# Performance work log

Measured on AMD Instinct MI355X. Metric: run time of the kernel, lower is better.

Reference implementation:

```python
import jax, jax.numpy as jnp
import numpy as np

N_NODES = 100000
N_EDGES = 1600000
IN_C, HID, N_CLS = 128, 128, 40


def setup_inputs() -> dict:
    key = jax.random.key(0)
    ks = jax.random.split(key, 8)
    x = jax.random.normal(ks[0], (N_NODES, IN_C), dtype=jnp.float32)
    edge_index = jax.random.randint(ks[1], (2, N_EDGES), 0, N_NODES, dtype=jnp.int64)
    s1 = 1.0 / np.sqrt(IN_C)
    s2 = 1.0 / np.sqrt(HID)
    return {
        "x": x,
        "edge_index": edge_index,
        "Wl1": jax.random.normal(ks[2], (IN_C, HID), dtype=jnp.float32) * s1,
        "Wr1": jax.random.normal(ks[3], (IN_C, HID), dtype=jnp.float32) * s1,
        "b1": jnp.zeros((HID,), dtype=jnp.float32),
        "Wl2": jax.random.normal(ks[4], (HID, N_CLS), dtype=jnp.float32) * s2,
        "Wr2": jax.random.normal(ks[5], (HID, N_CLS), dtype=jnp.float32) * s2,
        "b2": jnp.zeros((N_CLS,), dtype=jnp.float32),
    }


def _sage_conv(x, src, dst, Wl, Wr, b):
    # mean-aggregate neighbor features at destination nodes
    n = x.shape[0]
    agg = jax.ops.segment_sum(x[src], dst, num_segments=n)           # [N, C]
    cnt = jax.ops.segment_sum(jnp.ones((src.shape[0],), x.dtype), dst, num_segments=n)
    mean = agg / jnp.maximum(cnt, 1.0)[:, None]
    return mean @ Wl + x @ Wr + b


def reference(x, edge_index, Wl1, Wr1, b1, Wl2, Wr2, b2):
    src, dst = edge_index[0], edge_index[1]
    h = jax.nn.relu(_sage_conv(x, src, dst, Wl1, Wr1, b1))
    return _sage_conv(h, src, dst, Wl2, Wr2, b2)
```

## Files before the change

kernel.cpp:

```cpp
#include <hip/hip_runtime.h>

#define C_IN 128
#define N_CLS 40
#define ZB   40

#define NPB   256
#define MAXNB 512
#define CAP   6144
#define BCSTR 16

typedef __attribute__((ext_vector_type(8))) short bf16x8;
typedef __attribute__((ext_vector_type(4))) float f32x4;
typedef __attribute__((ext_vector_type(2))) float f32x2;

__device__ __forceinline__ ushort f2b(float f) {
  union { float f; unsigned u; } v; v.f = f;
  unsigned r = v.u + 0x7FFF + ((v.u >> 16) & 1);
  return (ushort)(r >> 16);
}
__device__ __forceinline__ unsigned packbf(float lo, float hi) {
  return (unsigned)f2b(lo) | ((unsigned)f2b(hi) << 16);
}
__device__ __forceinline__ void acc2(float& fa, float& fb, unsigned u) {
  union { unsigned u; float f; } lo, hi;
  lo.u = u << 16; hi.u = u & 0xFFFF0000u;
  fa += lo.f; fb += hi.f;
}

#if __has_builtin(__builtin_amdgcn_cvt_pk_f32_fp8) && __has_builtin(__builtin_amdgcn_cvt_pk_fp8_f32)
#define HW_FP8 1
#else
#define HW_FP8 0
#endif

__device__ __forceinline__ float f8dec1(unsigned b) {
  unsigned E = (b >> 3) & 15, M = b & 7;
  if (E) {
    union { unsigned u; float f; } v;
    v.u = ((b & 0x80u) << 24) | ((E + 120u) << 23) | (M << 20);
    return v.f;
  }
  float m = (float)(int)M * 0.001953125f;
  return (b & 0x80u) ? -m : m;
}
__device__ __forceinline__ unsigned f8enc1(float x) {
  union { float f; unsigned u; } v; v.f = x;
  unsigned s = (v.u >> 31) << 7;
  float ax = fabsf(x);
  if (ax < 9.765625e-4f) return s;
  if (ax < 0.015625f) {
    int M = (int)rintf(ax * 512.0f);
    return (M >= 8) ? (s | 0x08u) : (s | (unsigned)M);
  }
  if (ax > 448.0f) return s | 0x7Eu;
  unsigned au = v.u & 0x7FFFFFFFu;
  unsigned r = au + 0x7FFFFu + ((au >> 20) & 1);
  int e = (int)(r >> 23) - 127;
  unsigned M = (r >> 20) & 7;
  if (e > 8) return s | 0x7Eu;
  return s | ((unsigned)(e + 7) << 3) | M;
}
__device__ __forceinline__ void accf8x4(float* a, unsigned u) {
#if HW_FP8
  f32x2 lo = __builtin_amdgcn_cvt_pk_f32_fp8((int)u, false);
  f32x2 hi = __builtin_amdgcn_cvt_pk_f32_fp8((int)u, true);
  a[0] += lo[0]; a[1] += lo[1]; a[2] += hi[0]; a[3] += hi[1];
#else
  a[0] += f8dec1(u & 0xFF); a[1] += f8dec1((u >> 8) & 0xFF);
  a[2] += f8dec1((u >> 16) & 0xFF); a[3] += f8dec1(u >> 24);
#endif
}
__device__ __forceinline__ unsigned packf8x4(float x0, float x1, float x2, float x3) {
#if HW_FP8
  int p = 0;
  p = __builtin_amdgcn_cvt_pk_fp8_f32(x0, x1, p, false);
  p = __builtin_amdgcn_cvt_pk_fp8_f32(x2, x3, p, true);
  return (unsigned)p;
#else
  return f8enc1(x0) | (f8enc1(x1) << 8) | (f8enc1(x2) << 16) | (f8enc1(x3) << 24);
#endif
}
__device__ __forceinline__ unsigned char f8enc_byte(float x) {
#if HW_FP8
  return (unsigned char)(__builtin_amdgcn_cvt_pk_fp8_f32(x, x, 0, false) & 0xFF);
#else
  return (unsigned char)f8enc1(x);
#endif
}

__global__ __launch_bounds__(256) void bin_kernel(
    const int* __restrict__ src, const int* __restrict__ dst,
    int* __restrict__ bcur, unsigned* __restrict__ staged, int E, int NB)
{
  __shared__ int wcnt[4][MAXNB];
  __shared__ int wbase[4][MAXNB];
  const int tid = threadIdx.x;
  const int wv = tid >> 6;
  for (int i = tid; i < NB; i += 256) {
    wcnt[0][i] = 0; wcnt[1][i] = 0; wcnt[2][i] = 0; wcnt[3][i] = 0;
  }
  __syncthreads();
  const int e0 = blockIdx.x * 2048;
  const int eend = min(e0 + 2048, E);
  for (int e = e0 + tid; e < eend; e += 256)
    atomicAdd(&wcnt[wv][dst[e] >> 8], 1);
  __syncthreads();
  for (int i = tid; i < NB; i += 256) {
    int c0 = wcnt[0][i], c1 = wcnt[1][i], c2 = wcnt[2][i], c3 = wcnt[3][i];
    int tot = c0 + c1 + c2 + c3;
    int g = (tot > 0) ? atomicAdd(&bcur[i * BCSTR], tot) : 0;
    wbase[0][i] = g;
    wbase[1][i] = g + c0;
    wbase[2][i] = g + c0 + c1;
    wbase[3][i] = g + c0 + c1 + c2;
    wcnt[0][i] = 0; wcnt[1][i] = 0; wcnt[2][i] = 0; wcnt[3][i] = 0;
  }
  __syncthreads();
  for (int e = e0 + tid; e < eend; e += 256) {
    int d = dst[e];
    int b = d >> 8;
    int pos = wbase[wv][b] + atomicAdd(&wcnt[wv][b], 1);
    if (pos < CAP)
      staged[(size_t)b * CAP + pos] = (unsigned)src[e] | ((unsigned)(d & 255) << 20);
  }
}

__global__ __launch_bounds__(256) void csr_cvt_kernel(
    const unsigned* __restrict__ staged, const int* __restrict__ bcur,
    int* __restrict__ row_ptr, int* __restrict__ deg, int* __restrict__ csr_src,
    int N, int NB,
    const float* __restrict__ xin, ushort* __restrict__ xb,
    unsigned char* __restrict__ xf8, long n8)
{
  __shared__ unsigned st[CAP];
  __shared__ int dcnt[NPB];
  __shared__ int cur[NPB];
  __shared__ int wsum[4];
  __shared__ int rb_s;
  const int tid = threadIdx.x;
  if (blockIdx.x >= NB) {
    long i = ((long)(blockIdx.x - NB) * 256 + tid);
    if (i < n8) {
      const float4 a = *reinterpret_cast<const float4*>(xin + i * 8);
      const float4 b = *reinterpret_cast<const float4*>(xin + i * 8 + 4);
      uint4 o;
      o.x = packbf(a.x, a.y);
      o.y = packbf(a.z, a.w);
      o.z = packbf(b.x, b.y);
      o.w = packbf(b.z, b.w);
      *reinterpret_cast<uint4*>(xb + i * 8) = o;
      uint2 p;
      p.x = packf8x4(a.x, a.y, a.z, a.w);
      p.y = packf8x4(b.x, b.y, b.z, b.w);
      *reinterpret_cast<uint2*>(xf8 + i * 8) = p;
    }
    return;
  }
  const int b = blockIdx.x;
  const int cb = min(bcur[b * BCSTR], CAP);
  for (int i = tid; i < cb; i += 256) st[i] = staged[(size_t)b * CAP + i];
  int part = 0;
  for (int i = tid; i < b; i += 256) part += min(bcur[i * BCSTR], CAP);
  if (tid == 0) rb_s = 0;
  dcnt[tid] = 0;
  __syncthreads();
  #pragma unroll
  for (int off = 32; off > 0; off >>= 1) part += __shfl_down(part, off);
  if ((tid & 63) == 0 && part != 0) atomicAdd(&rb_s, part);
  for (int i = tid; i < cb; i += 256) atomicAdd(&dcnt[st[i] >> 20], 1);
  __syncthreads();
  const int rb = rb_s;
  int d = dcnt[tid];
  const int lane = tid & 63, w = tid >> 6;
  int inc = d;
  #pragma unroll
  for (int off = 1; off < 64; off <<= 1) {
    int v = __shfl_up(inc, off);
    if (lane >= off) inc += v;
  }
  if (lane == 63) wsum[w] = inc;
  __syncthreads();
  int wo = 0;
  for (int i = 0; i < w; ++i) wo += wsum[i];
  const int excl = wo + inc - d;
  cur[tid] = excl;
  const int node = b * NPB + tid;
  if (node < N) { row_ptr[node] = rb + excl; deg[node] = d; }
  __syncthreads();
  for (int i = tid; i < cb; i += 256) {
    unsigned wv = st[i];
    int p = atomicAdd(&cur[wv >> 20], 1);
    csr_src[rb + p] = (int)(wv & 0xFFFFF);
  }
}

__global__ __launch_bounds__(256) void agg1_kernel(
    const unsigned char* __restrict__ xf8, const ushort* __restrict__ xb,
    const int* __restrict__ csr_src, const int* __restrict__ row_ptr,
    const int* __restrict__ deg, ushort* __restrict__ mean, int N)
{
  int t = blockIdx.x * 256 + threadIdx.x;
  int n = t >> 3;
  if (n >= N) return;
  int q = t & 7;
  int base = row_ptr[n];
  int d = deg[n];
  float a[16];
  #pragma unroll
  for (int i = 0; i < 16; ++i) a[i] = 0.f;
  if (d > 8) {
    const unsigned char* fq = xf8 + q * 16;
    int j = 0;
    for (; j + 4 <= d; j += 4) {
      int s0 = csr_src[base + j + 0];
      int s1 = csr_src[base + j + 1];
      int s2 = csr_src[base + j + 2];
      int s3 = csr_src[base + j + 3];
      uint4 v0 = *reinterpret_cast<const uint4*>(fq + (size_t)s0 * C_IN);
      uint4 v1 = *reinterpret_cast<const uint4*>(fq + (size_t)s1 * C_IN);
      uint4 v2 = *reinterpret_cast<const uint4*>(fq + (size_t)s2 * C_IN);
      uint4 v3 = *reinterpret_cast<const uint4*>(fq + (size_t)s3 * C_IN);
      accf8x4(a+0, v0.x); accf8x4(a+4, v0.y); accf8x4(a+8, v0.z); accf8x4(a+12, v0.w);
      accf8x4(a+0, v1.x); accf8x4(a+4, v1.y); accf8x4(a+8, v1.z); accf8x4(a+12, v1.w);
      accf8x4(a+0, v2.x); accf8x4(a+4, v2.y); accf8x4(a+8, v2.z); accf8x4(a+12, v2.w);
      accf8x4(a+0, v3.x); accf8x4(a+4, v3.y); accf8x4(a+8, v3.z); accf8x4(a+12, v3.w);
    }
    for (; j < d; ++j) {
      int s = csr_src[base + j];
      uint4 v = *reinterpret_cast<const uint4*>(fq + (size_t)s * C_IN);
      accf8x4(a+0, v.x); accf8x4(a+4, v.y); accf8x4(a+8, v.z); accf8x4(a+12, v.w);
    }
  } else {
    const ushort* fq = xb + q * 16;
    for (int j = 0; j < d; ++j) {
      int s = csr_src[base + j];
      uint4 w0 = *reinterpret_cast<const uint4*>(fq + (size_t)s * C_IN);
      uint4 w1 = *reinterpret_cast<const uint4*>(fq + (size_t)s * C_IN + 8);
      acc2(a[0],a[1],w0.x); acc2(a[2],a[3],w0.y); acc2(a[4],a[5],w0.z); acc2(a[6],a[7],w0.w);
      acc2(a[8],a[9],w1.x); acc2(a[10],a[11],w1.y); acc2(a[12],a[13],w1.z); acc2(a[14],a[15],w1.w);
    }
  }
  float inv = (d > 0) ? (1.0f / (float)d) : 0.0f;
  uint4 o0, o1;
  o0.x = packbf(a[0]*inv, a[1]*inv);  o0.y = packbf(a[2]*inv, a[3]*inv);
  o0.z = packbf(a[4]*inv, a[5]*inv);  o0.w = packbf(a[6]*inv, a[7]*inv);
  o1.x = packbf(a[8]*inv, a[9]*inv);  o1.y = packbf(a[10]*inv, a[11]*inv);
  o1.z = packbf(a[12]*inv, a[13]*inv); o1.w = packbf(a[14]*inv, a[15]*inv);
  uint4* mp = reinterpret_cast<uint4*>(mean + (size_t)n * C_IN + q * 16);
  mp[0] = o0;
  mp[1] = o1;
}

__global__ __launch_bounds__(256) void layer1_mfma(
    const ushort* __restrict__ xb, const ushort* __restrict__ mb,
    const float* __restrict__ Wr, const float* __restrict__ Wl,
    const float* __restrict__ bias, ushort* __restrict__ h, int N, int ntiles)
{
  __shared__ ushort sB[8 * 8 * 64 * 8];
  const int tid = threadIdx.x;
  for (int idx = tid; idx < 8 * 8 * 64; idx += 256) {
    int l  = idx & 63;
    int cg = (idx >> 6) & 7;
    int ks = idx >> 9;
    int c  = cg * 16 + (l & 15);
    int kb = ks * 32 + 8 * (l >> 4);
    ushort* p = &sB[idx * 8];
    #pragma unroll
    for (int j = 0; j < 8; ++j) {
      int k = kb + j;
      float w = (k < C_IN) ? Wr[k * C_IN + c] : Wl[(k - C_IN) * C_IN + c];
      p[j] = f2b(w);
    }
  }
  __syncthreads();
  const int w = tid >> 6, l = tid & 63;
  const int rfrag = l & 15, kg = l >> 4;
  for (int tile = blockIdx.x; tile < ntiles; tile += gridDim.x) {
    int n0 = tile * 128 + w * 32;
    int rc0 = n0 + rfrag;      rc0 = (rc0 < N) ? rc0 : (N - 1);
    int rc1 = n0 + 16 + rfrag; rc1 = (rc1 < N) ? rc1 : (N - 1);
    f32x4 acc[2][8] = {};
    #pragma unroll
    for (int ks = 0; ks < 8; ++ks) {
      int kb = ks * 32 + kg * 8;
      const ushort* Asrc = (kb < C_IN) ? (xb + kb) : (mb + (kb - C_IN));
      bf16x8 a0 = *reinterpret_cast<const bf16x8*>(Asrc + (size_t)rc0 * C_IN);
      bf16x8 a1 = *reinterpret_cast<const bf16x8*>(Asrc + (size_t)rc1 * C_IN);
      #pragma unroll
      for (int cg = 0; cg < 8; ++cg) {
        bf16x8 b = *reinterpret_cast<const bf16x8*>(&sB[((ks * 8 + cg) * 64 + l) * 8]);
        acc[0][cg] = __builtin_amdgcn_mfma_f32_16x16x32_bf16(a0, b, acc[0][cg], 0, 0, 0);
        acc[1][cg] = __builtin_amdgcn_mfma_f32_16x16x32_bf16(a1, b, acc[1][cg], 0, 0, 0);
      }
    }
    const int rowoff = (l >> 4) * 4, colbase = l & 15;
    #pragma unroll
    for (int f = 0; f < 2; ++f) {
      #pragma unroll
      for (int cg = 0; cg < 8; ++cg) {
        int c = cg * 16 + colbase;
        float bc = bias[c];
        #pragma unroll
        for (int r = 0; r < 4; ++r) {
          int row = n0 + f * 16 + rowoff + r;
          if (row < N) {
            float v = fmaxf(acc[f][cg][r] + bc, 0.0f);
            h[(size_t)row * C_IN + c] = f2b(v);
          }
        }
      }
    }
  }
}

__global__ __launch_bounds__(256) void gemm2_dual(
    const ushort* __restrict__ hb,
    const float* __restrict__ Wl, const float* __restrict__ Wr,
    unsigned char* __restrict__ z, float* __restrict__ out, int N, int ntiles)
{
  __shared__ ushort sBl[4 * 3 * 64 * 8];
  __shared__ ushort sBr[4 * 3 * 64 * 8];
  const int tid = threadIdx.x;
  for (int idx = tid; idx < 4 * 3 * 64; idx += 256) {
    int l  = idx & 63;
    int cg = (idx >> 6) % 3;
    int ks = idx / (3 * 64);
    int c  = cg * 16 + (l & 15);
    int kb = ks * 32 + 8 * (l >> 4);
    ushort* pl = &sBl[idx * 8];
    ushort* pr = &sBr[idx * 8];
    #pragma unroll
    for (int j = 0; j < 8; ++j) {
      int k = kb + j;
      float wl = 0.0f, wr = 0.0f;
      if (c < N_CLS) { wl = Wl[k * N_CLS + c]; wr = Wr[k * N_CLS + c]; }
      pl[j] = f2b(wl);
      pr[j] = f2b(wr);
    }
  }
  __syncthreads();
  const int w = tid >> 6, l = tid & 63;
  const int rfrag = l & 15, kg = l >> 4;
  for (int tile = blockIdx.x; tile < ntiles; tile += gridDim.x) {
    int n0 = tile * 128 + w * 32;
    int rc0 = n0 + rfrag;      rc0 = (rc0 < N) ? rc0 : (N - 1);
    int rc1 = n0 + 16 + rfrag; rc1 = (rc1 < N) ? rc1 : (N - 1);
    f32x4 az[2][3] = {};
    f32x4 ay[2][3] = {};
    #pragma unroll
    for (int ks = 0; ks < 4; ++ks) {
      int kb = ks * 32 + kg * 8;
      bf16x8 a0 = *reinterpret_cast<const bf16x8*>(hb + (size_t)rc0 * C_IN + kb);
      bf16x8 a1 = *reinterpret_cast<const bf16x8*>(hb + (size_t)rc1 * C_IN + kb);
      #pragma unroll
      for (int cg = 0; cg < 3; ++cg) {
        bf16x8 bl = *reinterpret_cast<const bf16x8*>(&sBl[((ks * 3 + cg) * 64 + l) * 8]);
        bf16x8 br = *reinterpret_cast<const bf16x8*>(&sBr[((ks * 3 + cg) * 64 + l) * 8]);
        az[0][cg] = __builtin_amdgcn_mfma_f32_16x16x32_bf16(a0, bl, az[0][cg], 0, 0, 0);
        az[1][cg] = __builtin_amdgcn_mfma_f32_16x16x32_bf16(a1, bl, az[1][cg], 0, 0, 0);
        ay[0][cg] = __builtin_amdgcn_mfma_f32_16x16x32_bf16(a0, br, ay[0][cg], 0, 0, 0);
        ay[1][cg] = __builtin_amdgcn_mfma_f32_16x16x32_bf16(a1, br, ay[1][cg], 0, 0, 0);
      }
    }
    const int rowoff = (l >> 4) * 4, colbase = l & 15;
    #pragma unroll
    for (int f = 0; f < 2; ++f) {
      #pragma unroll
      for (int cg = 0; cg < 3; ++cg) {
        int c = cg * 16 + colbase;
        if (c < N_CLS) {
          #pragma unroll
          for (int r = 0; r < 4; ++r) {
            int row = n0 + f * 16 + rowoff + r;
            if (row < N) {
              z[(size_t)row * ZB + c] = f8enc_byte(az[f][cg][r]);
              out[(size_t)row * N_CLS + c] = ay[f][cg][r];
            }
          }
        }
      }
    }
  }
}

__global__ __launch_bounds__(256) void agg2z_kernel(
    const unsigned char* __restrict__ z, const int* __restrict__ csr_src,
    const int* __restrict__ row_ptr, const int* __restrict__ deg,
    const float* __restrict__ b2, float* __restrict__ out, int N)
{
  unsigned w = blockIdx.x * 256 + threadIdx.x;
  unsigned n = w / 5u;
  if (n >= (unsigned)N) return;
  unsigned q = w - n * 5u;
  const unsigned char* zq = z + q * 8;
  int base = row_ptr[n];
  int d = deg[n];
  float a[8];
  #pragma unroll
  for (int i = 0; i < 8; ++i) a[i] = 0.f;
  int j = 0;
  for (; j + 4 <= d; j += 4) {
    int s0 = csr_src[base + j + 0];
    int s1 = csr_src[base + j + 1];
    int s2 = csr_src[base + j + 2];
    int s3 = csr_src[base + j + 3];
    uint2 v0 = *reinterpret_cast<const uint2*>(zq + (size_t)s0 * ZB);
    uint2 v1 = *reinterpret_cast<const uint2*>(zq + (size_t)s1 * ZB);
    uint2 v2 = *reinterpret_cast<const uint2*>(zq + (size_t)s2 * ZB);
    uint2 v3 = *reinterpret_cast<const uint2*>(zq + (size_t)s3 * ZB);
    accf8x4(a+0, v0.x); accf8x4(a+4, v0.y);
    accf8x4(a+0, v1.x); accf8x4(a+4, v1.y);
    accf8x4(a+0, v2.x); accf8x4(a+4, v2.y);
    accf8x4(a+0, v3.x); accf8x4(a+4, v3.y);
  }
  for (; j < d; ++j) {
    int s = csr_src[base + j];
    uint2 v = *reinterpret_cast<const uint2*>(zq + (size_t)s * ZB);
    accf8x4(a+0, v.x); accf8x4(a+4, v.y);
  }
  float inv = (d > 0) ? (1.0f / (float)d) : 0.0f;
  float* op = out + (size_t)n * N_CLS + q * 8;
  const float4 bA = *reinterpret_cast<const float4*>(b2 + q * 8);
  const float4 bB = *reinterpret_cast<const float4*>(b2 + q * 8 + 4);
  float4 y0 = *reinterpret_cast<const float4*>(op);
  float4 y1 = *reinterpret_cast<const float4*>(op + 4);
  y0.x += a[0] * inv + bA.x; y0.y += a[1] * inv + bA.y;
  y0.z += a[2] * inv + bA.z; y0.w += a[3] * inv + bA.w;
  y1.x += a[4] * inv + bB.x; y1.y += a[5] * inv + bB.y;
  y1.z += a[6] * inv + bB.z; y1.w += a[7] * inv + bB.w;
  *reinterpret_cast<float4*>(op) = y0;
  *reinterpret_cast<float4*>(op + 4) = y1;
}

extern "C" void kernel_launch(void* const* d_in, const int* in_sizes, int n_in,
                              void* d_out, int out_size, void* d_ws, size_t ws_size,
                              hipStream_t stream)
{
  const float* x   = (const float*)d_in[0];
  const int*   ei  = (const int*)d_in[1];
  const float* Wl1 = (const float*)d_in[2];
  const float* Wr1 = (const float*)d_in[3];
  const float* b1  = (const float*)d_in[4];
  const float* Wl2 = (const float*)d_in[5];
  const float* Wr2 = (const float*)d_in[6];
  const float* b2  = (const float*)d_in[7];
  float* out = (float*)d_out;

  const int N = in_sizes[0] / C_IN;
  const int E = in_sizes[1] / 2;
  const int* src = ei;
  const int* dst = ei + E;
  const int NB = (N + NPB - 1) / NPB;

  size_t Np = ((size_t)N + 255) & ~(size_t)255;
  size_t Ep = ((size_t)E + 255) & ~(size_t)255;
  int* wsi     = (int*)d_ws;
  int* bcur    = wsi;
  int* row_ptr = wsi + (size_t)MAXNB * BCSTR;
  int* deg     = row_ptr + Np;
  int* csr_src = deg + Np;
  unsigned* staged = (unsigned*)(csr_src + Ep);
  unsigned char* zb = (unsigned char*)staged;
  ushort* xb    = (ushort*)(staged + (size_t)MAXNB * CAP);
  ushort* meanb = xb + (size_t)N * C_IN;
  ushort* hb    = meanb + (size_t)N * C_IN;
  unsigned char* xf8 = (unsigned char*)(hb + (size_t)N * C_IN);

  hipMemsetAsync(bcur, 0, (size_t)MAXNB * BCSTR * sizeof(int), stream);

  const int nbin = (E + 2047) / 2048;
  bin_kernel<<<nbin, 256, 0, stream>>>(src, dst, bcur, staged, E, NB);

  long n8 = (long)N * C_IN / 8;
  const int ncvt = (int)((n8 + 255) / 256);
  csr_cvt_kernel<<<NB + ncvt, 256, 0, stream>>>(staged, bcur, row_ptr, deg, csr_src,
                                                N, NB, x, xb, xf8, n8);

  const int ntiles = (N + 127) / 128;

  agg1_kernel<<<(N * 8 + 255) / 256, 256, 0, stream>>>(xf8, xb, csr_src, row_ptr, deg, meanb, N);
  layer1_mfma<<<512, 256, 0, stream>>>(xb, meanb, Wr1, Wl1, b1, hb, N, ntiles);

  gemm2_dual<<<512, 256, 0, stream>>>(hb, Wl2, Wr2, zb, out, N, ntiles);
  agg2z_kernel<<<(N * 5 + 255) / 256, 256, 0, stream>>>(zb, csr_src, row_ptr, deg, b2, out, N);
}
```

Measured before the change: 188.5 us.

## Fuse x conversion into edge binning kernel and enlarge bin chunks

The bf16/fp8 conversion of x now runs in the same launch as the edge binning kernel rather than alongside CSR construction. Each binning block now handles 8192 edges instead of 2048, caches the packed edge words and bin ids in shared memory so dst/src are read only once, and uses one shared counter set instead of four per-wave sets. The goal is fewer global atomics on bcur, no second read of the edge arrays, and better overlap of the conversion work with the binning. In exchange there are fewer binning blocks, more shared-memory use per block, and more contention on the shared-memory atomics.

New measurement: 170.8 us. -9.4%, faster.

```diff
diff --git a/kernel.cpp b/kernel.cpp
--- a/kernel.cpp
+++ b/kernel.cpp
@@ -8,6 +8,7 @@
 #define MAXNB 512
 #define CAP   6144
 #define BCSTR 16
+#define BINB  8192
 
 typedef __attribute__((ext_vector_type(8))) short bf16x8;
 typedef __attribute__((ext_vector_type(4))) float f32x4;
@@ -88,58 +89,19 @@
 #endif
 }
 
-__global__ __launch_bounds__(256) void bin_kernel(
+__global__ __launch_bounds__(256) void bin_cvt_kernel(
     const int* __restrict__ src, const int* __restrict__ dst,
-    int* __restrict__ bcur, unsigned* __restrict__ staged, int E, int NB)
-{
-  __shared__ int wcnt[4][MAXNB];
-  __shared__ int wbase[4][MAXNB];
-  const int tid = threadIdx.x;
-  const int wv = tid >> 6;
-  for (int i = tid; i < NB; i += 256) {
-    wcnt[0][i] = 0; wcnt[1][i] = 0; wcnt[2][i] = 0; wcnt[3][i] = 0;
-  }
-  __syncthreads();
-  const int e0 = blockIdx.x * 2048;
-  const int eend = min(e0 + 2048, E);
-  for (int e = e0 + tid; e < eend; e += 256)
-    atomicAdd(&wcnt[wv][dst[e] >> 8], 1);
-  __syncthreads();
-  for (int i = tid; i < NB; i += 256) {
-    int c0 = wcnt[0][i], c1 = wcnt[1][i], c2 = wcnt[2][i], c3 = wcnt[3][i];
-    int tot = c0 + c1 + c2 + c3;
-    int g = (tot > 0) ? atomicAdd(&bcur[i * BCSTR], tot) : 0;
-    wbase[0][i] = g;
-    wbase[1][i] = g + c0;
-    wbase[2][i] = g + c0 + c1;
-    wbase[3][i] = g + c0 + c1 + c2;
-    wcnt[0][i] = 0; wcnt[1][i] = 0; wcnt[2][i] = 0; wcnt[3][i] = 0;
-  }
-  __syncthreads();
-  for (int e = e0 + tid; e < eend; e += 256) {
-    int d = dst[e];
-    int b = d >> 8;
-    int pos = wbase[wv][b] + atomicAdd(&wcnt[wv][b], 1);
-    if (pos < CAP)
-      staged[(size_t)b * CAP + pos] = (unsigned)src[e] | ((unsigned)(d & 255) << 20);
-  }
-}
-
-__global__ __launch_bounds__(256) void csr_cvt_kernel(
-    const unsigned* __restrict__ staged, const int* __restrict__ bcur,
-    int* __restrict__ row_ptr, int* __restrict__ deg, int* __restrict__ csr_src,
-    int N, int NB,
+    int* __restrict__ bcur, unsigned* __restrict__ staged, int E, int NB, int nbin,
     const float* __restrict__ xin, ushort* __restrict__ xb,
     unsigned char* __restrict__ xf8, long n8)
 {
-  __shared__ unsigned st[CAP];
-  __shared__ int dcnt[NPB];
-  __shared__ int cur[NPB];
-  __shared__ int wsum[4];
-  __shared__ int rb_s;
+  __shared__ unsigned sw[BINB];
+  __shared__ ushort  sb[BINB];
+  __shared__ int cnt[MAXNB];
+  __shared__ int base[MAXNB];
   const int tid = threadIdx.x;
-  if (blockIdx.x >= NB) {
-    long i = ((long)(blockIdx.x - NB) * 256 + tid);
+  if (blockIdx.x >= nbin) {
+    long i = ((long)(blockIdx.x - nbin) * 256 + tid);
     if (i < n8) {
       const float4 a = *reinterpret_cast<const float4*>(xin + i * 8);
       const float4 b = *reinterpret_cast<const float4*>(xin + i * 8 + 4);
@@ -156,7 +118,43 @@
     }
     return;
   }
-  const int b = blockIdx.x;
+  for (int i = tid; i < NB; i += 256) cnt[i] = 0;
+  __syncthreads();
+  const int e0 = blockIdx.x * BINB;
+  const int nE = min(BINB, E - e0);
+  for (int k = tid; k < nE; k += 256) {
+    int d = dst[e0 + k];
+    int s = src[e0 + k];
+    int b = d >> 8;
+    sw[k] = (unsigned)s | ((unsigned)(d & 255) << 20);
+    sb[k] = (ushort)b;
+    atomicAdd(&cnt[b], 1);
+  }
+  __syncthreads();
+  for (int i = tid; i < NB; i += 256) {
+    int c = cnt[i];
+    base[i] = (c > 0) ? atomicAdd(&bcur[i * BCSTR], c) : 0;
+    cnt[i] = 0;
+  }
+  __syncthreads();
+  for (int k = tid; k < nE; k += 256) {
+    int b = sb[k];
+    int pos = base[b] + atomicAdd(&cnt[b], 1);
+    if (pos < CAP)
+      staged[(size_t)b * CAP + pos] = sw[k];
+  }
+}
+
+__global__ __launch_bounds__(256) void csr_kernel(
+    const unsigned* __restrict__ staged, const int* __restrict__ bcur,
+    int* __restrict__ row_ptr, int* __restrict__ deg, int* __restrict__ csr_src, int N)
+{
+  __shared__ unsigned st[CAP];
+  __shared__ int dcnt[NPB];
+  __shared__ int cur[NPB];
+  __shared__ int wsum[4];
+  __shared__ int rb_s;
+  const int b = blockIdx.x, tid = threadIdx.x;
   const int cb = min(bcur[b * BCSTR], CAP);
   for (int i = tid; i < cb; i += 256) st[i] = staged[(size_t)b * CAP + i];
   int part = 0;
@@ -468,13 +466,13 @@
 
   hipMemsetAsync(bcur, 0, (size_t)MAXNB * BCSTR * sizeof(int), stream);
 
-  const int nbin = (E + 2047) / 2048;
-  bin_kernel<<<nbin, 256, 0, stream>>>(src, dst, bcur, staged, E, NB);
-
+  const int nbin = (E + BINB - 1) / BINB;
   long n8 = (long)N * C_IN / 8;
   const int ncvt = (int)((n8 + 255) / 256);
-  csr_cvt_kernel<<<NB + ncvt, 256, 0, stream>>>(staged, bcur, row_ptr, deg, csr_src,
-                                                N, NB, x, xb, xf8, n8);
+  bin_cvt_kernel<<<nbin + ncvt, 256, 0, stream>>>(src, dst, bcur, staged, E, NB, nbin,
+                                                  x, xb, xf8, n8);
+
+  csr_kernel<<<NB, 256, 0, stream>>>(staged, bcur, row_ptr, deg, csr_src, N);
 
   const int ntiles = (N + 127) / 128;
 
```
